# Kernel optimization log

Hardware: AMD Instinct MI355X
Metric: run time of the kernel (lower is better)

Reference implementation:

```python
import jax, jax.numpy as jnp
import numpy as np

B, S, HID = 2, 2048, 2048
NH, HD = 16, 128
KVC, QC = 512, 1536


def _rope(x):
    # x: [B, H, S, D]; interleaved-pair rotation matching the torch view(..., D//2, 2)
    b, h, s, d = x.shape
    inv_freq = 1.0 / (10000.0 ** (jnp.arange(0, d, 2, dtype=jnp.float32) / d))  # [D/2]
    pos = jnp.arange(s, dtype=jnp.float32)
    sinusoid = pos[:, None] * inv_freq[None, :]  # [S, D/2]
    sin = jnp.sin(sinusoid)[None, None]  # [1,1,S,D/2]
    cos = jnp.cos(sinusoid)[None, None]
    xr = x.reshape(b, h, s, d // 2, 2)
    x1, x2 = xr[..., 0], xr[..., 1]
    out = jnp.stack([x1 * cos - x2 * sin, x1 * sin + x2 * cos], axis=-1)
    return out.reshape(b, h, s, d)


def setup_inputs() -> dict:
    key = jax.random.key(0)
    ks = jax.random.split(key, 14)
    def lin(k, fan_in, fan_out):
        lim = 1.0 / np.sqrt(fan_in)
        kw, kb = jax.random.split(k)
        W = jax.random.uniform(kw, (fan_in, fan_out), jnp.float32, -lim, lim)
        b = jax.random.uniform(kb, (fan_out,), jnp.float32, -lim, lim)
        return W, b
    x = jax.random.normal(ks[0], (B, S, HID), jnp.float32)
    # causal mask (positions with 0 are masked out)
    attention_mask = jnp.tril(jnp.ones((S, S), jnp.int32))[None, None]  # [1,1,S,S]
    W_dkv, b_dkv = lin(ks[1], HID, KVC)
    W_uk, b_uk = lin(ks[2], KVC, NH * HD)
    W_uv, b_uv = lin(ks[3], KVC, NH * HD)
    W_dq, b_dq = lin(ks[4], HID, QC)
    W_uq, b_uq = lin(ks[5], QC, NH * HD)
    W_o, b_o = lin(ks[6], NH * HD, HID)
    return dict(x=x, attention_mask=attention_mask,
                W_dkv=W_dkv, b_dkv=b_dkv, W_uk=W_uk, b_uk=b_uk,
                W_uv=W_uv, b_uv=b_uv, W_dq=W_dq, b_dq=b_dq,
                W_uq=W_uq, b_uq=b_uq, W_o=W_o, b_o=b_o)


def reference(x, attention_mask, W_dkv, b_dkv, W_uk, b_uk, W_uv, b_uv,
              W_dq, b_dq, W_uq, b_uq, W_o, b_o):
    b, s, _ = x.shape
    kv = x @ W_dkv + b_dkv                                   # [B,S,KVC]
    k = (kv @ W_uk + b_uk).reshape(b, s, NH, HD).transpose(0, 2, 1, 3)  # [B,H,S,D]
    v = (kv @ W_uv + b_uv).reshape(b, s, NH, HD).transpose(0, 2, 1, 3)
    q = ((x @ W_dq + b_dq) @ W_uq + b_uq).reshape(b, s, NH, HD).transpose(0, 2, 1, 3)
    q, k = _rope(q), _rope(k)
    scores = jnp.einsum('bhqd,bhkd->bhqk', q, k) / jnp.sqrt(jnp.float32(HD))
    scores = jnp.where(attention_mask == 0, jnp.float32(-1e9), scores)
    probs = jax.nn.softmax(scores, axis=-1)
    out = jnp.einsum('bhqk,bhkd->bhqd', probs, v)            # [B,H,S,D]
    out = out.transpose(0, 2, 1, 3).reshape(b, s, NH * HD)
    return out @ W_o + b_o
```

## Files before the change

kernel.cpp:

```cpp
#include <hip/hip_runtime.h>
#include <stdint.h>

typedef unsigned short u16;
typedef uint32_t u32;
typedef __attribute__((ext_vector_type(8))) short short8;
typedef __attribute__((ext_vector_type(4))) float f32x4;
typedef __attribute__((ext_vector_type(4))) u32 u32x4;
typedef __attribute__((ext_vector_type(2))) u32 u32x2;
typedef __attribute__((ext_vector_type(4))) unsigned short u16x4;

#define BS_ 4096
#define S_ 2048
#define HID_ 2048

__device__ __forceinline__ float bf2f(u16 u) { union { u32 i; float f; } v; v.i = ((u32)u) << 16; return v.f; }
__device__ __forceinline__ u16 f2bf(float f) {
  union { float f; u32 i; } v; v.f = f;
  u32 r = v.i + 0x7fffu + ((v.i >> 16) & 1u);
  return (u16)(r >> 16);
}

__device__ __forceinline__ void gload16(const void* gsrc, void* ldst) {
  __builtin_amdgcn_global_load_lds(
      (const __attribute__((address_space(1))) void*)gsrc,
      (__attribute__((address_space(3))) void*)ldst, 16, 0, 0);
}

__global__ __launch_bounds__(256) void conv_f2b(const float* __restrict__ in, u16* __restrict__ out, int n4) {
  int i = blockIdx.x * 256 + threadIdx.x;
  if (i < n4) {
    float4 v = ((const float4*)in)[i];
    u16x4 o;
    o.x = f2bf(v.x); o.y = f2bf(v.y); o.z = f2bf(v.z); o.w = f2bf(v.w);
    ((u16x4*)out)[i] = o;
  }
}

__global__ __launch_bounds__(256) void transpose_conv(const float* __restrict__ W, u16* __restrict__ WT,
                                                      int K, int N) {
  __shared__ float tile[64][65];
  const int t = threadIdx.x;
  const int kb = blockIdx.y * 64, nb = blockIdx.x * 64;
#pragma unroll
  for (int c = 0; c < 4; ++c) {
    int idx = c * 256 + t;
    int row = idx >> 4;
    int col4 = (idx & 15) * 4;
    float4 v = *(const float4*)&W[(size_t)(kb + row) * N + nb + col4];
    tile[row][col4 + 0] = v.x; tile[row][col4 + 1] = v.y;
    tile[row][col4 + 2] = v.z; tile[row][col4 + 3] = v.w;
  }
  __syncthreads();
#pragma unroll
  for (int c = 0; c < 4; ++c) {
    int idx = c * 256 + t;
    int n = idx >> 4;
    int k4 = (idx & 15) * 4;
    u16x4 o;
    o.x = f2bf(tile[k4 + 0][n]); o.y = f2bf(tile[k4 + 1][n]);
    o.z = f2bf(tile[k4 + 2][n]); o.w = f2bf(tile[k4 + 3][n]);
    *(u16x4*)&WT[(size_t)(nb + n) * K + kb + k4] = o;
  }
}

__global__ __launch_bounds__(256) void concat_bias(const float* __restrict__ b_dkv, const float* __restrict__ b_dq,
                                                   const float* __restrict__ b_uk, const float* __restrict__ b_uv,
                                                   float* __restrict__ bc1, float* __restrict__ bc2) {
  int i = blockIdx.x * 256 + threadIdx.x;
  if (i < 512) bc1[i] = b_dkv[i];
  else if (i < 2048) bc1[i] = b_dq[i - 512];
  else if (i < 4096) bc2[i - 2048] = b_uk[i - 2048];
  else if (i < 6144) bc2[i - 2048] = b_uv[i - 4096];
}

__global__ __launch_bounds__(256) void vtrans(const u16* __restrict__ KVin, u16* __restrict__ VT) {
  __shared__ u16 tile[64][136];
  const int t = threadIdx.x;
  const int st0 = blockIdx.x * 64;
  const int bh = blockIdx.y;
  const int bb = bh >> 4, h = bh & 15;
  const u16* src = KVin + (size_t)bb * S_ * 4096 + 2048 + (size_t)h * 128;
  u16* dst = VT + (size_t)bh * 128 * S_;
#pragma unroll
  for (int c = 0; c < 4; ++c) {
    int idx = c * 256 + t;
    int s = idx >> 4, ch = idx & 15;
    short8 v = *(const short8*)&src[(size_t)(st0 + s) * 4096 + ch * 8];
    *(short8*)&tile[s][ch * 8] = v;
  }
  __syncthreads();
#pragma unroll
  for (int c = 0; c < 4; ++c) {
    int idx = c * 256 + t;
    int d = idx >> 3, ch = idx & 7;
    short8 o;
#pragma unroll
    for (int j = 0; j < 8; ++j) o[j] = tile[ch * 8 + j][d];
    *(short8*)&dst[(size_t)d * S_ + st0 + ch * 8] = o;
  }
}

__global__ __launch_bounds__(256) void rope_table(float* __restrict__ cs) {
  int idx = blockIdx.x * 256 + threadIdx.x;
  int pos = idx >> 6, i = idx & 63;
  float inv = powf(10000.f, -(float)i / 64.f);
  float a = (float)pos * inv;
  cs[idx * 2] = cosf(a);
  cs[idx * 2 + 1] = sinf(a);
}

template <int OUTF32, int ROPE>
__global__ __launch_bounds__(256) void gemm_bt(const u16* __restrict__ A, int lda,
                                               const u16* __restrict__ BT,
                                               const float* __restrict__ bias,
                                               const float* __restrict__ cs,
                                               void* __restrict__ Cout,
                                               int M, int N, int K) {
  __shared__ u16 As[128 * 64];
  __shared__ u16 Bs[128 * 64];
  const int t = threadIdx.x;
  const int lane = t & 63, wave = t >> 6;
  const int wm = wave >> 1, wn = wave & 1;
  const int gx = gridDim.x;
  const int nwg = gx * gridDim.y;
  const int flat = blockIdx.y * gx + blockIdx.x;
  const int swz = (flat & 7) * (nwg >> 3) + (flat >> 3);
  const int tn = swz % gx, tm = swz / gx;
  const int r16 = lane & 15, q4 = lane >> 4;

  f32x4 acc[4][4];
#pragma unroll
  for (int m = 0; m < 4; ++m)
#pragma unroll
    for (int n = 0; n < 4; ++n) acc[m][n] = (f32x4){0.f, 0.f, 0.f, 0.f};

  for (int kt = 0; kt < K; kt += 64) {
#pragma unroll
    for (int c = 0; c < 4; ++c) {
      int idx = c * 256 + t;
      int row = idx >> 3, ch = idx & 7;
      gload16(&A[(size_t)(tm * 128 + row) * lda + kt + ch * 8], (char*)As + idx * 16);
      gload16(&BT[(size_t)(tn * 128 + row) * K + kt + ch * 8], (char*)Bs + idx * 16);
    }
    __syncthreads();
#pragma unroll
    for (int kk = 0; kk < 64; kk += 32) {
      short8 af[4], bfv[4];
#pragma unroll
      for (int m = 0; m < 4; ++m)
        af[m] = *(const short8*)&As[(wm * 64 + m * 16 + r16) * 64 + kk + q4 * 8];
#pragma unroll
      for (int n = 0; n < 4; ++n)
        bfv[n] = *(const short8*)&Bs[(wn * 64 + n * 16 + r16) * 64 + kk + q4 * 8];
      __builtin_amdgcn_s_setprio(1);
#pragma unroll
      for (int m = 0; m < 4; ++m)
#pragma unroll
        for (int n = 0; n < 4; ++n)
          acc[m][n] = __builtin_amdgcn_mfma_f32_16x16x32_bf16(bfv[n], af[m], acc[m][n], 0, 0, 0);
      __builtin_amdgcn_s_setprio(0);
    }
    __syncthreads();
  }
#pragma unroll
  for (int n = 0; n < 4; ++n) {
    int gc0 = tn * 128 + wn * 64 + n * 16 + q4 * 4;
    float4 bv4 = *(const float4*)&bias[gc0];
    const int i0 = (gc0 & 127) >> 1;
#pragma unroll
    for (int m = 0; m < 4; ++m) {
      int grow = tm * 128 + wm * 64 + m * 16 + r16;
      float v0 = acc[m][n][0] + bv4.x, v1 = acc[m][n][1] + bv4.y;
      float v2 = acc[m][n][2] + bv4.z, v3 = acc[m][n][3] + bv4.w;
      if (ROPE && gc0 < ROPE) {
        int s = grow & 2047;
        float4 cp = *(const float4*)&cs[((size_t)s * 64 + i0) * 2];
        float y0 = v0 * cp.x - v1 * cp.y;
        float y1 = v0 * cp.y + v1 * cp.x;
        float y2 = v2 * cp.z - v3 * cp.w;
        float y3 = v2 * cp.w + v3 * cp.z;
        v0 = y0; v1 = y1; v2 = y2; v3 = y3;
      }
      if (OUTF32) {
        float4 o; o.x = v0; o.y = v1; o.z = v2; o.w = v3;
        *(float4*)&((float*)Cout)[(size_t)grow * N + gc0] = o;
      } else {
        u16x4 o; o.x = f2bf(v0); o.y = f2bf(v1); o.z = f2bf(v2); o.w = f2bf(v3);
        *(u16x4*)&((u16*)Cout)[(size_t)grow * N + gc0] = o;
      }
    }
  }
}

__global__ __launch_bounds__(256, 2) void attn_kernel(const u16* __restrict__ Q, const u16* __restrict__ K,
                                                      int kld, const u16* __restrict__ VT,
                                                      u16* __restrict__ O) {
  __shared__ char smem[75776];
  u16* Kl = (u16*)smem;
  u16* Vl = (u16*)(smem + 32768);
  u16* Pl = (u16*)(smem + 65536);
  float* ex = (float*)smem;

  const int t = threadIdx.x;
  const int lane = t & 63, w = t >> 6;
  const int r16 = lane & 15, q4 = lane >> 4;
  const int par = w >> 1, sub = w & 1;
  const int b = blockIdx.x;
  const int xcd = b & 7, u = b >> 3;
  const int p = u & 15, g4 = u >> 4;
  const int bh = g4 * 8 + xcd;
  const int bb = bh >> 4, h = bh & 15;
  const u16* Qb = Q + (size_t)bb * S_ * HID_ + (size_t)h * 128;
  const u16* Kb = K + (size_t)bb * S_ * kld + (size_t)h * 128;
  const u16* VTb = VT + (size_t)bh * 128 * S_;
  u16* Ob = O + (size_t)bb * S_ * HID_ + (size_t)h * 128;

  auto stage = [&](int rs, int kvbase) {
#pragma unroll
    for (int pp = 0; pp < 2; ++pp) {
      int kvb = kvbase + pp * 32;
      char* kd = (char*)(Kl + (size_t)(rs * 2 + pp) * 4096);
      char* vd = (char*)(Vl + (size_t)(rs * 2 + pp) * 4096);
#pragma unroll
      for (int c = 0; c < 2; ++c) {
        int s = c * 256 + t;
        int row = s >> 4;
        int ch = (s & 15) ^ (row & 7);
        gload16(&Kb[(size_t)(kvb + row) * kld + ch * 8], kd + s * 16);
      }
#pragma unroll
      for (int c = 0; c < 2; ++c) {
        int s = c * 256 + t;
        int row = s >> 2;
        int ch = (s & 3) ^ ((row >> 1) & 3);
        gload16(&VTb[(size_t)row * S_ + kvb + ch * 8], vd + s * 16);
      }
    }
  };

  u16* Pw = Pl + (size_t)w * 1280;
  const float SCALE = 0.08838834764831845f;

#pragma unroll
  for (int seg = 0; seg < 2; ++seg) {
    const int qt = seg ? (31 - p) : p;
    const int nr = qt + 1;
    const int qrow0 = qt * 64 + sub * 32;

    short8 qf[2][4];
#pragma unroll
    for (int m = 0; m < 2; ++m)
#pragma unroll
      for (int dk = 0; dk < 4; ++dk)
        qf[m][dk] = *(const short8*)&Qb[(size_t)(qrow0 + m * 16 + r16) * HID_ + dk * 32 + q4 * 8];

    f32x4 ao[2][8];
    float mr[2], lr[2];
#pragma unroll
    for (int m = 0; m < 2; ++m) {
#pragma unroll
      for (int dn = 0; dn < 8; ++dn) ao[m][dn] = (f32x4){0.f, 0.f, 0.f, 0.f};
      mr[m] = -1e30f; lr[m] = 0.f;
    }

    stage(0, 0);
    __syncthreads();

    for (int r = 0; r < nr; ++r) {
      const int rs = r & 1;
      if (r + 1 < nr) stage(rs ^ 1, (r + 1) * 64);
      const int kv0 = r * 64 + par * 32;
      const u16* Kbuf = Kl + (size_t)(rs * 2 + par) * 4096;
      const u16* Vbuf = Vl + (size_t)(rs * 2 + par) * 4096;

      if (kv0 <= qrow0 + 31) {
        f32x4 sc[2][2];
#pragma unroll
        for (int m = 0; m < 2; ++m)
#pragma unroll
          for (int n = 0; n < 2; ++n) sc[m][n] = (f32x4){0.f, 0.f, 0.f, 0.f};
#pragma unroll
        for (int dk = 0; dk < 4; ++dk) {
          short8 kf[2];
#pragma unroll
          for (int n = 0; n < 2; ++n) {
            int kr = n * 16 + r16;
            int ba = (kr * 256 + dk * 64 + q4 * 16) ^ ((kr & 7) << 4);
            kf[n] = *(const short8*)((const char*)Kbuf + ba);
          }
          __builtin_amdgcn_s_setprio(1);
#pragma unroll
          for (int n = 0; n < 2; ++n)
#pragma unroll
            for (int m = 0; m < 2; ++m)
              sc[m][n] = __builtin_amdgcn_mfma_f32_16x16x32_bf16(kf[n], qf[m][dk], sc[m][n], 0, 0, 0);
          __builtin_amdgcn_s_setprio(0);
        }
        const bool nm = (kv0 + 31 > qrow0);
#pragma unroll
        for (int m = 0; m < 2; ++m) {
          const int q = qrow0 + m * 16 + r16;
#pragma unroll
          for (int n = 0; n < 2; ++n)
#pragma unroll
            for (int j = 0; j < 4; ++j) {
              float sv = sc[m][n][j] * SCALE;
              if (nm) {
                int kv = kv0 + n * 16 + q4 * 4 + j;
                if (kv > q) sv = -1e30f;
              }
              sc[m][n][j] = sv;
            }
        }
        float tm0[2];
#pragma unroll
        for (int m = 0; m < 2; ++m) {
          float tm = sc[m][0][0];
#pragma unroll
          for (int n = 0; n < 2; ++n)
#pragma unroll
            for (int j = 0; j < 4; ++j) tm = fmaxf(tm, sc[m][n][j]);
          tm = fmaxf(tm, __shfl_xor(tm, 16));
          tm = fmaxf(tm, __shfl_xor(tm, 32));
          tm0[m] = tm;
        }
        float growth = fmaxf(tm0[0] - mr[0], tm0[1] - mr[1]);
        if (!__all(growth <= 8.0f)) {
#pragma unroll
          for (int m = 0; m < 2; ++m) {
            float mnew = fmaxf(mr[m], tm0[m]);
            float fsc = __expf(mr[m] - mnew);
            lr[m] *= fsc; mr[m] = mnew;
#pragma unroll
            for (int dn = 0; dn < 8; ++dn) ao[m][dn] *= fsc;
          }
        }
#pragma unroll
        for (int m = 0; m < 2; ++m) {
          float ps = 0.f;
#pragma unroll
          for (int n = 0; n < 2; ++n)
#pragma unroll
            for (int j = 0; j < 4; ++j) {
              float pv = __expf(sc[m][n][j] - mr[m]);
              sc[m][n][j] = pv;
              ps += pv;
            }
          ps += __shfl_xor(ps, 16);
          ps += __shfl_xor(ps, 32);
          lr[m] += ps;
        }
#pragma unroll
        for (int m = 0; m < 2; ++m)
#pragma unroll
          for (int n = 0; n < 2; ++n) {
            u32 lo, hi;
            asm("v_cvt_pk_bf16_f32 %0, %1, %2" : "=v"(lo) : "v"(sc[m][n][0]), "v"(sc[m][n][1]));
            asm("v_cvt_pk_bf16_f32 %0, %1, %2" : "=v"(hi) : "v"(sc[m][n][2]), "v"(sc[m][n][3]));
            u32x2 pr; pr.x = lo; pr.y = hi;
            int ba = (m * 16 + r16) * 80 + n * 32 + q4 * 8;
            *(u32x2*)((char*)Pw + ba) = pr;
          }
        short8 pb[2];
#pragma unroll
        for (int m = 0; m < 2; ++m)
          pb[m] = *(const short8*)((const char*)Pw + (m * 16 + r16) * 80 + q4 * 16);
        __builtin_amdgcn_s_setprio(1);
#pragma unroll
        for (int dn = 0; dn < 8; ++dn) {
          int d = dn * 16 + r16;
          int bv = d * 64 + ((q4 ^ ((d >> 1) & 3)) * 16);
          short8 vf = *(const short8*)((const char*)Vbuf + bv);
#pragma unroll
          for (int m = 0; m < 2; ++m)
            ao[m][dn] = __builtin_amdgcn_mfma_f32_16x16x32_bf16(vf, pb[m], ao[m][dn], 0, 0, 0);
        }
        __builtin_amdgcn_s_setprio(0);
      }
      __syncthreads();
    }

    {
      float* exb = ex + (size_t)sub * 4352 + (size_t)lane * 68;
      if (par == 1) {
#pragma unroll
        for (int m = 0; m < 2; ++m)
#pragma unroll
          for (int dn = 0; dn < 8; ++dn)
            *(f32x4*)(exb + m * 32 + dn * 4) = ao[m][dn];
        exb[64] = mr[0]; exb[65] = mr[1]; exb[66] = lr[0]; exb[67] = lr[1];
      }
      __syncthreads();
      if (par == 0) {
#pragma unroll
        for (int m = 0; m < 2; ++m) {
          float mB = exb[64 + m], lB = exb[66 + m];
          float mx = fmaxf(mr[m], mB);
          float wA = __expf(mr[m] - mx), wB = __expf(mB - mx);
          float inv = 1.f / (lr[m] * wA + lB * wB);
          const int q = qrow0 + m * 16 + r16;
#pragma unroll
          for (int dn = 0; dn < 8; ++dn) {
            f32x4 ob = *(const f32x4*)(exb + m * 32 + dn * 4);
            u16x4 o;
#pragma unroll
            for (int j = 0; j < 4; ++j) o[j] = f2bf((ao[m][dn][j] * wA + ob[j] * wB) * inv);
            *(u16x4*)&Ob[(size_t)q * HID_ + dn * 16 + q4 * 4] = o;
          }
        }
      }
      __syncthreads();
    }
  }
}

extern "C" void kernel_launch(void* const* d_in, const int* in_sizes, int n_in,
                              void* d_out, int out_size, void* d_ws, size_t ws_size,
                              hipStream_t stream) {
  (void)in_sizes; (void)n_in; (void)out_size; (void)ws_size;
  const float* x     = (const float*)d_in[0];
  const float* W_dkv = (const float*)d_in[2];
  const float* b_dkv = (const float*)d_in[3];
  const float* W_uk  = (const float*)d_in[4];
  const float* b_uk  = (const float*)d_in[5];
  const float* W_uv  = (const float*)d_in[6];
  const float* b_uv  = (const float*)d_in[7];
  const float* W_dq  = (const float*)d_in[8];
  const float* b_dq  = (const float*)d_in[9];
  const float* W_uq  = (const float*)d_in[10];
  const float* b_uq  = (const float*)d_in[11];
  const float* W_o   = (const float*)d_in[12];
  const float* b_o   = (const float*)d_in[13];
  float* out = (float*)d_out;

  char* ws = (char*)d_ws;
  size_t off = 0;
  auto carve = [&](size_t bytes) { void* p = ws + off; off += (bytes + 255) & ~(size_t)255; return p; };
  u16* xb     = (u16*)carve((size_t)BS_ * 2048 * 2);
  u16* WdkvqT = (u16*)carve((size_t)2048 * 2048 * 2);
  u16* WukvT  = (u16*)carve((size_t)4096 * 512 * 2);
  u16* WuqT   = (u16*)carve((size_t)2048 * 1536 * 2);
  u16* WoT    = (u16*)carve((size_t)2048 * 2048 * 2);
  u16* kvq1   = (u16*)carve((size_t)BS_ * 2048 * 2);
  u16* kvbuf  = (u16*)carve((size_t)BS_ * 4096 * 2);
  u16* qb     = (u16*)carve((size_t)BS_ * 2048 * 2);
  u16* aob    = (u16*)carve((size_t)BS_ * 2048 * 2);
  float* cs   = (float*)carve((size_t)2048 * 64 * 2 * 4);
  float* bc1  = (float*)carve((size_t)2048 * 4);
  float* bc2  = (float*)carve((size_t)4096 * 4);
  u16* VT     = xb;

  conv_f2b<<<dim3(BS_ * 2048 / 4 / 256), 256, 0, stream>>>(x, xb, BS_ * 2048 / 4);
  transpose_conv<<<dim3(512 / 64, 2048 / 64), 256, 0, stream>>>(W_dkv, WdkvqT, 2048, 512);
  transpose_conv<<<dim3(1536 / 64, 2048 / 64), 256, 0, stream>>>(W_dq, WdkvqT + (size_t)512 * 2048, 2048, 1536);
  transpose_conv<<<dim3(2048 / 64, 512 / 64), 256, 0, stream>>>(W_uk, WukvT, 512, 2048);
  transpose_conv<<<dim3(2048 / 64, 512 / 64), 256, 0, stream>>>(W_uv, WukvT + (size_t)2048 * 512, 512, 2048);
  transpose_conv<<<dim3(2048 / 64, 1536 / 64), 256, 0, stream>>>(W_uq, WuqT, 1536, 2048);
  transpose_conv<<<dim3(2048 / 64, 2048 / 64), 256, 0, stream>>>(W_o, WoT, 2048, 2048);
  rope_table<<<dim3(512), 256, 0, stream>>>(cs);
  concat_bias<<<dim3(24), 256, 0, stream>>>(b_dkv, b_dq, b_uk, b_uv, bc1, bc2);

  gemm_bt<0, 0><<<dim3(2048 / 128, BS_ / 128), 256, 0, stream>>>(xb, 2048, WdkvqT, bc1, nullptr, kvq1, BS_, 2048, 2048);
  gemm_bt<0, 2048><<<dim3(4096 / 128, BS_ / 128), 256, 0, stream>>>(kvq1, 2048, WukvT, bc2, cs, kvbuf, BS_, 4096, 512);
  gemm_bt<0, 2048><<<dim3(2048 / 128, BS_ / 128), 256, 0, stream>>>(kvq1 + 512, 2048, WuqT, b_uq, cs, qb, BS_, 2048, 1536);

  vtrans<<<dim3(S_ / 64, 32), 256, 0, stream>>>(kvbuf, VT);

  attn_kernel<<<dim3(512), 256, 0, stream>>>(qb, kvbuf, 4096, VT, aob);

  gemm_bt<1, 0><<<dim3(2048 / 128, BS_ / 128), 256, 0, stream>>>(aob, 2048, WoT, b_o, nullptr, out, BS_, 2048, 2048);
}
```

Baseline: 302.5 us.

## Merge prep kernels, fuse up-projection GEMMs, write V transposed from epilogue

Nine preprocessing launches (x conversion, weight transposes, rope table, bias concat) are merged into one multi-role prep kernel. The K/V and Q up-projection GEMMs now run in a single launch, which fills the device better. The V columns are written directly in transposed layout from the GEMM epilogue, so the separate vtrans kernel and the full KV buffer go away. The cost is scattered 2-byte strided stores for V, which may coalesce poorly.

```diff
diff --git a/kernel.cpp b/kernel.cpp
--- a/kernel.cpp
+++ b/kernel.cpp
@@ -26,94 +26,83 @@
       (__attribute__((address_space(3))) void*)ldst, 16, 0, 0);
 }
 
-__global__ __launch_bounds__(256) void conv_f2b(const float* __restrict__ in, u16* __restrict__ out, int n4) {
-  int i = blockIdx.x * 256 + threadIdx.x;
-  if (i < n4) {
-    float4 v = ((const float4*)in)[i];
+__global__ __launch_bounds__(256) void prep(const float* __restrict__ x, u16* __restrict__ xb,
+                                            const float* __restrict__ W_dkv, const float* __restrict__ W_dq,
+                                            const float* __restrict__ W_uk, const float* __restrict__ W_uv,
+                                            const float* __restrict__ W_uq, const float* __restrict__ W_o,
+                                            u16* __restrict__ WdkvqT, u16* __restrict__ WukvT,
+                                            u16* __restrict__ WuqT, u16* __restrict__ WoT,
+                                            const float* __restrict__ b_dkv, const float* __restrict__ b_dq,
+                                            const float* __restrict__ b_uk, const float* __restrict__ b_uv,
+                                            float* __restrict__ cs, float* __restrict__ bc1,
+                                            float* __restrict__ bc2) {
+  __shared__ float tile[64][65];
+  int b = blockIdx.x;
+  const int t = threadIdx.x;
+  if (b < 8192) {
+    int i = b * 256 + t;
+    float4 v = ((const float4*)x)[i];
     u16x4 o;
     o.x = f2bf(v.x); o.y = f2bf(v.y); o.z = f2bf(v.z); o.w = f2bf(v.w);
-    ((u16x4*)out)[i] = o;
-  }
-}
-
-__global__ __launch_bounds__(256) void transpose_conv(const float* __restrict__ W, u16* __restrict__ WT,
-                                                      int K, int N) {
-  __shared__ float tile[64][65];
-  const int t = threadIdx.x;
-  const int kb = blockIdx.y * 64, nb = blockIdx.x * 64;
-#pragma unroll
-  for (int c = 0; c < 4; ++c) {
-    int idx = c * 256 + t;
-    int row = idx >> 4;
-    int col4 = (idx & 15) * 4;
-    float4 v = *(const float4*)&W[(size_t)(kb + row) * N + nb + col4];
-    tile[row][col4 + 0] = v.x; tile[row][col4 + 1] = v.y;
-    tile[row][col4 + 2] = v.z; tile[row][col4 + 3] = v.w;
-  }
-  __syncthreads();
-#pragma unroll
-  for (int c = 0; c < 4; ++c) {
-    int idx = c * 256 + t;
-    int n = idx >> 4;
-    int k4 = (idx & 15) * 4;
-    u16x4 o;
-    o.x = f2bf(tile[k4 + 0][n]); o.y = f2bf(tile[k4 + 1][n]);
-    o.z = f2bf(tile[k4 + 2][n]); o.w = f2bf(tile[k4 + 3][n]);
-    *(u16x4*)&WT[(size_t)(nb + n) * K + kb + k4] = o;
-  }
-}
-
-__global__ __launch_bounds__(256) void concat_bias(const float* __restrict__ b_dkv, const float* __restrict__ b_dq,
-                                                   const float* __restrict__ b_uk, const float* __restrict__ b_uv,
-                                                   float* __restrict__ bc1, float* __restrict__ bc2) {
-  int i = blockIdx.x * 256 + threadIdx.x;
-  if (i < 512) bc1[i] = b_dkv[i];
-  else if (i < 2048) bc1[i] = b_dq[i - 512];
-  else if (i < 4096) bc2[i - 2048] = b_uk[i - 2048];
-  else if (i < 6144) bc2[i - 2048] = b_uv[i - 4096];
-}
-
-__global__ __launch_bounds__(256) void vtrans(const u16* __restrict__ KVin, u16* __restrict__ VT) {
-  __shared__ u16 tile[64][136];
-  const int t = threadIdx.x;
-  const int st0 = blockIdx.x * 64;
-  const int bh = blockIdx.y;
-  const int bb = bh >> 4, h = bh & 15;
-  const u16* src = KVin + (size_t)bb * S_ * 4096 + 2048 + (size_t)h * 128;
-  u16* dst = VT + (size_t)bh * 128 * S_;
-#pragma unroll
-  for (int c = 0; c < 4; ++c) {
-    int idx = c * 256 + t;
-    int s = idx >> 4, ch = idx & 15;
-    short8 v = *(const short8*)&src[(size_t)(st0 + s) * 4096 + ch * 8];
-    *(short8*)&tile[s][ch * 8] = v;
-  }
-  __syncthreads();
-#pragma unroll
-  for (int c = 0; c < 4; ++c) {
-    int idx = c * 256 + t;
-    int d = idx >> 3, ch = idx & 7;
-    short8 o;
-#pragma unroll
-    for (int j = 0; j < 8; ++j) o[j] = tile[ch * 8 + j][d];
-    *(short8*)&dst[(size_t)d * S_ + st0 + ch * 8] = o;
-  }
-}
-
-__global__ __launch_bounds__(256) void rope_table(float* __restrict__ cs) {
-  int idx = blockIdx.x * 256 + threadIdx.x;
-  int pos = idx >> 6, i = idx & 63;
-  float inv = powf(10000.f, -(float)i / 64.f);
-  float a = (float)pos * inv;
-  cs[idx * 2] = cosf(a);
-  cs[idx * 2 + 1] = sinf(a);
-}
-
-template <int OUTF32, int ROPE>
+    ((u16x4*)xb)[i] = o;
+    return;
+  }
+  b -= 8192;
+  if (b < 3328) {
+    const float* W; u16* WT; int K, N, gx, r = b;
+    if (r < 256)                 { W = W_dkv; WT = WdkvqT;                    K = 2048; N = 512;  gx = 8;  }
+    else if ((r -= 256) < 768)   { W = W_dq;  WT = WdkvqT + (size_t)512 * 2048; K = 2048; N = 1536; gx = 24; }
+    else if ((r -= 768) < 256)   { W = W_uk;  WT = WukvT;                     K = 512;  N = 2048; gx = 32; }
+    else if ((r -= 256) < 256)   { W = W_uv;  WT = WukvT + (size_t)2048 * 512;  K = 512;  N = 2048; gx = 32; }
+    else if ((r -= 256) < 768)   { W = W_uq;  WT = WuqT;                      K = 1536; N = 2048; gx = 32; }
+    else                         { r -= 768;  W = W_o; WT = WoT;              K = 2048; N = 2048; gx = 32; }
+    const int nb = (r % gx) * 64, kb = (r / gx) * 64;
+#pragma unroll
+    for (int c = 0; c < 4; ++c) {
+      int idx = c * 256 + t;
+      int row = idx >> 4;
+      int col4 = (idx & 15) * 4;
+      float4 v = *(const float4*)&W[(size_t)(kb + row) * N + nb + col4];
+      tile[row][col4 + 0] = v.x; tile[row][col4 + 1] = v.y;
+      tile[row][col4 + 2] = v.z; tile[row][col4 + 3] = v.w;
+    }
+    __syncthreads();
+#pragma unroll
+    for (int c = 0; c < 4; ++c) {
+      int idx = c * 256 + t;
+      int n = idx >> 4;
+      int k4 = (idx & 15) * 4;
+      u16x4 o;
+      o.x = f2bf(tile[k4 + 0][n]); o.y = f2bf(tile[k4 + 1][n]);
+      o.z = f2bf(tile[k4 + 2][n]); o.w = f2bf(tile[k4 + 3][n]);
+      *(u16x4*)&WT[(size_t)(nb + n) * K + kb + k4] = o;
+    }
+    return;
+  }
+  b -= 3328;
+  if (b < 512) {
+    int idx = b * 256 + t;
+    int pos = idx >> 6, i = idx & 63;
+    float inv = powf(10000.f, -(float)i / 64.f);
+    float a = (float)pos * inv;
+    cs[idx * 2] = cosf(a);
+    cs[idx * 2 + 1] = sinf(a);
+    return;
+  }
+  b -= 512;
+  {
+    int i = b * 256 + t;
+    if (i < 512) bc1[i] = b_dkv[i];
+    else if (i < 2048) bc1[i] = b_dq[i - 512];
+    else if (i < 4096) bc2[i - 2048] = b_uk[i - 2048];
+    else if (i < 6144) bc2[i - 2048] = b_uv[i - 4096];
+  }
+}
+
+template <int OUTF32>
 __global__ __launch_bounds__(256) void gemm_bt(const u16* __restrict__ A, int lda,
                                                const u16* __restrict__ BT,
                                                const float* __restrict__ bias,
-                                               const float* __restrict__ cs,
                                                void* __restrict__ Cout,
                                                int M, int N, int K) {
   __shared__ u16 As[128 * 64];
@@ -166,27 +155,112 @@
   for (int n = 0; n < 4; ++n) {
     int gc0 = tn * 128 + wn * 64 + n * 16 + q4 * 4;
     float4 bv4 = *(const float4*)&bias[gc0];
-    const int i0 = (gc0 & 127) >> 1;
 #pragma unroll
     for (int m = 0; m < 4; ++m) {
       int grow = tm * 128 + wm * 64 + m * 16 + r16;
       float v0 = acc[m][n][0] + bv4.x, v1 = acc[m][n][1] + bv4.y;
       float v2 = acc[m][n][2] + bv4.z, v3 = acc[m][n][3] + bv4.w;
-      if (ROPE && gc0 < ROPE) {
+      if (OUTF32) {
+        float4 o; o.x = v0; o.y = v1; o.z = v2; o.w = v3;
+        *(float4*)&((float*)Cout)[(size_t)grow * N + gc0] = o;
+      } else {
+        u16x4 o; o.x = f2bf(v0); o.y = f2bf(v1); o.z = f2bf(v2); o.w = f2bf(v3);
+        *(u16x4*)&((u16*)Cout)[(size_t)grow * N + gc0] = o;
+      }
+    }
+  }
+}
+
+__global__ __launch_bounds__(256) void gemm23(const u16* __restrict__ kvq1,
+                                              const u16* __restrict__ WukvT, const u16* __restrict__ WuqT,
+                                              const float* __restrict__ bc2, const float* __restrict__ b_uq,
+                                              const float* __restrict__ cs,
+                                              u16* __restrict__ kbuf, u16* __restrict__ VT,
+                                              u16* __restrict__ qb) {
+  __shared__ u16 As[128 * 64];
+  __shared__ u16 Bs[128 * 64];
+  const int t = threadIdx.x;
+  const int lane = t & 63, wave = t >> 6;
+  const int wm = wave >> 1, wn = wave & 1;
+  const int bflat = blockIdx.x;
+  const bool g2 = (bflat < 1024);
+  const u16* A  = g2 ? kvq1 : (kvq1 + 512);
+  const u16* BT = g2 ? WukvT : WuqT;
+  const float* bias = g2 ? bc2 : b_uq;
+  const int N = g2 ? 4096 : 2048;
+  const int K = g2 ? 512 : 1536;
+  const int gx = g2 ? 32 : 16;
+  const int nwg = g2 ? 1024 : 512;
+  const int flat = g2 ? bflat : (bflat - 1024);
+  const int swz = (flat & 7) * (nwg >> 3) + (flat >> 3);
+  const int tn = swz % gx, tm = swz / gx;
+  const int r16 = lane & 15, q4 = lane >> 4;
+
+  f32x4 acc[4][4];
+#pragma unroll
+  for (int m = 0; m < 4; ++m)
+#pragma unroll
+    for (int n = 0; n < 4; ++n) acc[m][n] = (f32x4){0.f, 0.f, 0.f, 0.f};
+
+  for (int kt = 0; kt < K; kt += 64) {
+#pragma unroll
+    for (int c = 0; c < 4; ++c) {
+      int idx = c * 256 + t;
+      int row = idx >> 3, ch = idx & 7;
+      gload16(&A[(size_t)(tm * 128 + row) * 2048 + kt + ch * 8], (char*)As + idx * 16);
+      gload16(&BT[(size_t)(tn * 128 + row) * K + kt + ch * 8], (char*)Bs + idx * 16);
+    }
+    __syncthreads();
+#pragma unroll
+    for (int kk = 0; kk < 64; kk += 32) {
+      short8 af[4], bfv[4];
+#pragma unroll
+      for (int m = 0; m < 4; ++m)
+        af[m] = *(const short8*)&As[(wm * 64 + m * 16 + r16) * 64 + kk + q4 * 8];
+#pragma unroll
+      for (int n = 0; n < 4; ++n)
+        bfv[n] = *(const short8*)&Bs[(wn * 64 + n * 16 + r16) * 64 + kk + q4 * 8];
+      __builtin_amdgcn_s_setprio(1);
+#pragma unroll
+      for (int m = 0; m < 4; ++m)
+#pragma unroll
+        for (int n = 0; n < 4; ++n)
+          acc[m][n] = __builtin_amdgcn_mfma_f32_16x16x32_bf16(bfv[n], af[m], acc[m][n], 0, 0, 0);
+      __builtin_amdgcn_s_setprio(0);
+    }
+    __syncthreads();
+  }
+
+  const bool isV = g2 && (tn >= 16);
+  u16* outp = g2 ? kbuf : qb;
+#pragma unroll
+  for (int n = 0; n < 4; ++n) {
+    int gc0 = tn * 128 + wn * 64 + n * 16 + q4 * 4;
+    float4 bv4 = *(const float4*)&bias[gc0];
+    const int i0 = (gc0 & 127) >> 1;
+#pragma unroll
+    for (int m = 0; m < 4; ++m) {
+      int grow = tm * 128 + wm * 64 + m * 16 + r16;
+      float v0 = acc[m][n][0] + bv4.x, v1 = acc[m][n][1] + bv4.y;
+      float v2 = acc[m][n][2] + bv4.z, v3 = acc[m][n][3] + bv4.w;
+      if (!isV) {
         int s = grow & 2047;
         float4 cp = *(const float4*)&cs[((size_t)s * 64 + i0) * 2];
         float y0 = v0 * cp.x - v1 * cp.y;
         float y1 = v0 * cp.y + v1 * cp.x;
         float y2 = v2 * cp.z - v3 * cp.w;
         float y3 = v2 * cp.w + v3 * cp.z;
-        v0 = y0; v1 = y1; v2 = y2; v3 = y3;
-      }
-      if (OUTF32) {
-        float4 o; o.x = v0; o.y = v1; o.z = v2; o.w = v3;
-        *(float4*)&((float*)Cout)[(size_t)grow * N + gc0] = o;
+        u16x4 o; o.x = f2bf(y0); o.y = f2bf(y1); o.z = f2bf(y2); o.w = f2bf(y3);
+        *(u16x4*)&outp[(size_t)grow * 2048 + gc0] = o;
       } else {
-        u16x4 o; o.x = f2bf(v0); o.y = f2bf(v1); o.z = f2bf(v2); o.w = f2bf(v3);
-        *(u16x4*)&((u16*)Cout)[(size_t)grow * N + gc0] = o;
+        int gcv = gc0 - 2048;
+        int hh = gcv >> 7, d0 = gcv & 127;
+        int bb = grow >> 11, s = grow & 2047;
+        u16* vdst = VT + ((size_t)(bb * 16 + hh) * 128 + d0) * S_ + s;
+        vdst[0]        = f2bf(v0);
+        vdst[S_]       = f2bf(v1);
+        vdst[2 * S_]   = f2bf(v2);
+        vdst[3 * S_]   = f2bf(v3);
       }
     }
   }
@@ -442,7 +516,7 @@
   u16* WuqT   = (u16*)carve((size_t)2048 * 1536 * 2);
   u16* WoT    = (u16*)carve((size_t)2048 * 2048 * 2);
   u16* kvq1   = (u16*)carve((size_t)BS_ * 2048 * 2);
-  u16* kvbuf  = (u16*)carve((size_t)BS_ * 4096 * 2);
+  u16* kbuf   = (u16*)carve((size_t)BS_ * 2048 * 2);
   u16* qb     = (u16*)carve((size_t)BS_ * 2048 * 2);
   u16* aob    = (u16*)carve((size_t)BS_ * 2048 * 2);
   float* cs   = (float*)carve((size_t)2048 * 64 * 2 * 4);
@@ -450,23 +524,15 @@
   float* bc2  = (float*)carve((size_t)4096 * 4);
   u16* VT     = xb;
 
-  conv_f2b<<<dim3(BS_ * 2048 / 4 / 256), 256, 0, stream>>>(x, xb, BS_ * 2048 / 4);
-  transpose_conv<<<dim3(512 / 64, 2048 / 64), 256, 0, stream>>>(W_dkv, WdkvqT, 2048, 512);
-  transpose_conv<<<dim3(1536 / 64, 2048 / 64), 256, 0, stream>>>(W_dq, WdkvqT + (size_t)512 * 2048, 2048, 1536);
-  transpose_conv<<<dim3(2048 / 64, 512 / 64), 256, 0, stream>>>(W_uk, WukvT, 512, 2048);
-  transpose_conv<<<dim3(2048 / 64, 512 / 64), 256, 0, stream>>>(W_uv, WukvT + (size_t)2048 * 512, 512, 2048);
-  transpose_conv<<<dim3(2048 / 64, 1536 / 64), 256, 0, stream>>>(W_uq, WuqT, 1536, 2048);
-  transpose_conv<<<dim3(2048 / 64, 2048 / 64), 256, 0, stream>>>(W_o, WoT, 2048, 2048);
-  rope_table<<<dim3(512), 256, 0, stream>>>(cs);
-  concat_bias<<<dim3(24), 256, 0, stream>>>(b_dkv, b_dq, b_uk, b_uv, bc1, bc2);
-
-  gemm_bt<0, 0><<<dim3(2048 / 128, BS_ / 128), 256, 0, stream>>>(xb, 2048, WdkvqT, bc1, nullptr, kvq1, BS_, 2048, 2048);
-  gemm_bt<0, 2048><<<dim3(4096 / 128, BS_ / 128), 256, 0, stream>>>(kvq1, 2048, WukvT, bc2, cs, kvbuf, BS_, 4096, 512);
-  gemm_bt<0, 2048><<<dim3(2048 / 128, BS_ / 128), 256, 0, stream>>>(kvq1 + 512, 2048, WuqT, b_uq, cs, qb, BS_, 2048, 1536);
-
-  vtrans<<<dim3(S_ / 64, 32), 256, 0, stream>>>(kvbuf, VT);
-
-  attn_kernel<<<dim3(512), 256, 0, stream>>>(qb, kvbuf, 4096, VT, aob);
-
-  gemm_bt<1, 0><<<dim3(2048 / 128, BS_ / 128), 256, 0, stream>>>(aob, 2048, WoT, b_o, nullptr, out, BS_, 2048, 2048);
-}
+  prep<<<dim3(12056), 256, 0, stream>>>(x, xb, W_dkv, W_dq, W_uk, W_uv, W_uq, W_o,
+                                        WdkvqT, WukvT, WuqT, WoT,
+                                        b_dkv, b_dq, b_uk, b_uv, cs, bc1, bc2);
+
+  gemm_bt<0><<<dim3(2048 / 128, BS_ / 128), 256, 0, stream>>>(xb, 2048, WdkvqT, bc1, kvq1, BS_, 2048, 2048);
+
+  gemm23<<<dim3(1536), 256, 0, stream>>>(kvq1, WukvT, WuqT, bc2, b_uq, cs, kbuf, VT, qb);
+
+  attn_kernel<<<dim3(512), 256, 0, stream>>>(qb, kbuf, 2048, VT, aob);
+
+  gemm_bt<1><<<dim3(2048 / 128, BS_ / 128), 256, 0, stream>>>(aob, 2048, WoT, b_o, out, BS_, 2048, 2048);
+}
```

Result: faster. 271.3 us (-10.3%).
